# Performance work log

Hardware: AMD Instinct MI355X
Metric: run time of the kernel (lower is better)

## Reference

```python
import jax, jax.numpy as jnp
import numpy as np

B, L1, L2 = 16, 32, 128
DEC = 512       # decoder_size
MEM = 512       # memory_bank_size
TOP = 50        # topic_num


def setup_inputs() -> dict:
    key = jax.random.key(0)
    ks = jax.random.split(key, 16)
    s = lambda fan_in: 1.0 / np.sqrt(fan_in)
    inp = {
        "decoder_state": jax.random.normal(ks[0], (B, DEC), jnp.float32),
        "doc_memory": jax.random.normal(ks[1], (B, L1, MEM), jnp.float32),
        "word_memory": jax.random.normal(ks[2], (B, L1, L2, MEM), jnp.float32),
        "topic_dist": jax.random.uniform(ks[3], (B, TOP), jnp.float32),
        "doc_mask": jnp.ones((B, L1), jnp.int32),
        "word_mask": jnp.ones((B, L1, L2), jnp.int32),
        # HierAttention params (PyTorch Linear weight layout: [out, in])
        "Wv": jax.random.uniform(ks[4], (1, DEC), jnp.float32, -s(DEC), s(DEC)),
        "Wd": jax.random.uniform(ks[5], (DEC, DEC), jnp.float32, -s(DEC), s(DEC)),
        "Wt": jax.random.uniform(ks[6], (DEC, TOP), jnp.float32, -s(TOP), s(TOP)),
        "Wm": jax.random.uniform(ks[7], (DEC, MEM), jnp.float32, -s(MEM), s(MEM)),
        # doc_attention (inner Attention) params
        "Wv2": jax.random.uniform(ks[8], (1, DEC), jnp.float32, -s(DEC), s(DEC)),
        "Wd2": jax.random.uniform(ks[9], (DEC, DEC), jnp.float32, -s(DEC), s(DEC)),
        "Wt2": jax.random.uniform(ks[10], (DEC, TOP), jnp.float32, -s(TOP), s(TOP)),
        "Wm2": jax.random.uniform(ks[11], (DEC, MEM), jnp.float32, -s(MEM), s(MEM)),
    }
    return inp


def reference(decoder_state, doc_memory, word_memory, topic_dist,
              doc_mask, word_mask,
              Wv, Wd, Wt, Wm, Wv2, Wd2, Wt2, Wm2):
    neg_inf = jnp.float32(-jnp.inf)

    # ---- word-level (HierAttention.score) ----
    enc_feat = jnp.einsum('bqwm,dm->bqwd', word_memory, Wm)      # [B,L1,L2,DEC]
    dec_feat = decoder_state @ Wd.T                              # [B,DEC]
    top_feat = topic_dist @ Wt.T                                 # [B,DEC]
    e = jnp.tanh(enc_feat + (dec_feat + top_feat)[:, None, None, :])
    word_scores = jnp.einsum('bqwd,od->bqw', e, Wv)[..., 0] if Wv.shape[0] != 1 else jnp.einsum('bqwd,d->bqw', e, Wv[0])
    word_scores = jnp.where(word_mask == 0, neg_inf, word_scores)
    word_attn = jax.nn.softmax(word_scores, axis=-1)             # [B,L1,L2]

    # ---- doc-level (Attention.score) ----
    enc_feat_d = jnp.einsum('bqm,dm->bqd', doc_memory, Wm2)      # [B,L1,DEC]
    dec_feat_d = decoder_state @ Wd2.T                           # [B,DEC]
    top_feat_d = topic_dist @ Wt2.T                              # [B,DEC]
    e_d = jnp.tanh(enc_feat_d + (dec_feat_d + top_feat_d)[:, None, :])
    doc_scores = jnp.einsum('bqd,d->bq', e_d, Wv2[0])            # [B,L1]
    doc_scores = jnp.where(doc_mask == 0, neg_inf, doc_scores)
    doc_attn = jax.nn.softmax(doc_scores, axis=-1)               # [B,L1]

    # ---- combine ----
    rescaled = doc_attn[..., None] * word_attn                   # [B,L1,L2]
    context = jnp.einsum('bqw,bqwm->bm', rescaled, word_memory)  # [B,MEM]
    return context, rescaled
```

## Files before the change

### kernel.cpp

```cpp
#include <hip/hip_runtime.h>
#include <hip/hip_bf16.h>
#include <math.h>

#define BATCH 16
#define L1 32
#define L2 128
#define DEC 512
#define MEM 512
#define TOPN 50
#define NROWS (BATCH * L1 * L2)
#define NBQ (BATCH * L1)

typedef short short8 __attribute__((ext_vector_type(8)));
typedef float f32x16 __attribute__((ext_vector_type(16)));

#define WS_WP     0
#define WS_BIAS1  262144
#define WS_BIAS2  270336
#define WS_DOCSC  278528

__device__ __forceinline__ unsigned int pkbf(float a, float b) {
    __hip_bfloat162 h = __float22bfloat162_rn(float2{a, b});
    union { __hip_bfloat162 h; unsigned int u; } c{h};
    return c.u;
}

__device__ __forceinline__ float fast_tanh(float x) {
    return 1.f - 2.f / (__expf(2.f * x) + 1.f);
}

__device__ __forceinline__ float wave_sum64(float v) {
    v += __shfl_xor(v, 1);
    v += __shfl_xor(v, 2);
    v += __shfl_xor(v, 4);
    v += __shfl_xor(v, 8);
    v += __shfl_xor(v, 16);
    v += __shfl_xor(v, 32);
    return v;
}

__global__ __launch_bounds__(256) void setup_kernel(
    const float* __restrict__ Wm,
    unsigned short* __restrict__ Wp,
    const float* __restrict__ dec, const float* __restrict__ topic,
    const float* __restrict__ Wd, const float* __restrict__ Wt,
    const float* __restrict__ Wd2, const float* __restrict__ Wt2,
    float* __restrict__ bias1, float* __restrict__ bias2,
    float* __restrict__ ctx_out)
{
    const int bid = blockIdx.x;
    const int tid = threadIdx.x;
    if (bid < 128) {
        int s = bid * 256 + tid;
        int C = s >> 10;
        int u = s & 1023;
        int nt = u >> 6, k8 = (u >> 5) & 1, n_in = u & 31;
        int d = nt * 32 + n_in;
        int k = C * 16 + k8 * 8;

        const float4* src = (const float4*)(Wm + (size_t)d * DEC + k);
        float4 v0 = src[0], v1 = src[1];
        uint4 v;
        v.x = pkbf(v0.x, v0.y); v.y = pkbf(v0.z, v0.w);
        v.z = pkbf(v1.x, v1.y); v.w = pkbf(v1.z, v1.w);
        ((uint4*)Wp)[s] = v;
    } else if (bid < 128 + 4096) {
        int gw = (bid - 128) * 4 + (tid >> 6);
        int lane = tid & 63;
        int mat = gw >> 13;
        int rem = gw & 8191;
        int bb = rem >> 9;
        int d = rem & 511;

        const float* wrow = (mat ? Wd2 : Wd) + (size_t)d * DEC;
        const float* drow = dec + (size_t)bb * DEC;
        float4 a0 = ((const float4*)wrow)[lane * 2];
        float4 a1 = ((const float4*)wrow)[lane * 2 + 1];
        float4 x0 = ((const float4*)drow)[lane * 2];
        float4 x1 = ((const float4*)drow)[lane * 2 + 1];
        float acc = a0.x * x0.x;
        acc = fmaf(a0.y, x0.y, acc);
        acc = fmaf(a0.z, x0.z, acc);
        acc = fmaf(a0.w, x0.w, acc);
        acc = fmaf(a1.x, x1.x, acc);
        acc = fmaf(a1.y, x1.y, acc);
        acc = fmaf(a1.z, x1.z, acc);
        acc = fmaf(a1.w, x1.w, acc);
        const float* trow = (mat ? Wt2 : Wt) + (size_t)d * TOPN;
        if (lane < TOPN) acc = fmaf(trow[lane], topic[bb * TOPN + lane], acc);
#pragma unroll
        for (int o = 1; o <= 32; o <<= 1) acc += __shfl_xor(acc, o);
        if (lane == 0) (mat ? bias2 : bias1)[bb * DEC + d] = acc;
    } else {
        int i = (bid - (128 + 4096)) * 256 + tid;
        float4 z = {0.f, 0.f, 0.f, 0.f};
        ((float4*)ctx_out)[i * 2] = z;
        ((float4*)ctx_out)[i * 2 + 1] = z;
    }
}

__global__ __launch_bounds__(512) void doc_score_kernel(
    const float* __restrict__ Xd,
    const float* __restrict__ Wm2,
    const float* __restrict__ Wv2,
    const float* __restrict__ bias2,
    float* __restrict__ doc_scores)
{
    __shared__ float wsum[2][8];
    const int tid = threadIdx.x;
    const int lane = tid & 63;
    const int w = tid >> 6;
    const int row0 = blockIdx.x * 2;
    const int b = row0 >> 5;

    const float4* X0 = (const float4*)(Xd + (size_t)row0 * MEM) + lane * 2;
    const float4* X1 = (const float4*)(Xd + (size_t)(row0 + 1) * MEM) + lane * 2;
    float4 xa0 = X0[0], xb0 = X0[1];
    float4 xa1 = X1[0], xb1 = X1[1];

    float s0 = 0.f, s1 = 0.f;
#pragma unroll 2
    for (int dd = 0; dd < 64; dd += 2) {
        const int d = w * 64 + dd;
        const float4* W0 = (const float4*)(Wm2 + (size_t)d * MEM) + lane * 2;
        const float4* W1 = (const float4*)(Wm2 + (size_t)(d + 1) * MEM) + lane * 2;
        float4 wa0 = W0[0], wb0 = W0[1];
        float4 wa1 = W1[0], wb1 = W1[1];

        float p00 = wa0.x * xa0.x, p01 = wa1.x * xa0.x;
        float p10 = wa0.x * xa1.x, p11 = wa1.x * xa1.x;
        p00 = fmaf(wa0.y, xa0.y, p00); p01 = fmaf(wa1.y, xa0.y, p01);
        p10 = fmaf(wa0.y, xa1.y, p10); p11 = fmaf(wa1.y, xa1.y, p11);
        p00 = fmaf(wa0.z, xa0.z, p00); p01 = fmaf(wa1.z, xa0.z, p01);
        p10 = fmaf(wa0.z, xa1.z, p10); p11 = fmaf(wa1.z, xa1.z, p11);
        p00 = fmaf(wa0.w, xa0.w, p00); p01 = fmaf(wa1.w, xa0.w, p01);
        p10 = fmaf(wa0.w, xa1.w, p10); p11 = fmaf(wa1.w, xa1.w, p11);
        p00 = fmaf(wb0.x, xb0.x, p00); p01 = fmaf(wb1.x, xb0.x, p01);
        p10 = fmaf(wb0.x, xb1.x, p10); p11 = fmaf(wb1.x, xb1.x, p11);
        p00 = fmaf(wb0.y, xb0.y, p00); p01 = fmaf(wb1.y, xb0.y, p01);
        p10 = fmaf(wb0.y, xb1.y, p10); p11 = fmaf(wb1.y, xb1.y, p11);
        p00 = fmaf(wb0.z, xb0.z, p00); p01 = fmaf(wb1.z, xb0.z, p01);
        p10 = fmaf(wb0.z, xb1.z, p10); p11 = fmaf(wb1.z, xb1.z, p11);
        p00 = fmaf(wb0.w, xb0.w, p00); p01 = fmaf(wb1.w, xb0.w, p01);
        p10 = fmaf(wb0.w, xb1.w, p10); p11 = fmaf(wb1.w, xb1.w, p11);

        p00 = wave_sum64(p00);
        p01 = wave_sum64(p01);
        p10 = wave_sum64(p10);
        p11 = wave_sum64(p11);
        if (lane == 0) {
            float wva = Wv2[d], wvb = Wv2[d + 1];
            float bsa = bias2[b * DEC + d], bsb = bias2[b * DEC + d + 1];
            s0 += fmaf(wva, fast_tanh(p00 + bsa), wvb * fast_tanh(p01 + bsb));
            s1 += fmaf(wva, fast_tanh(p10 + bsa), wvb * fast_tanh(p11 + bsb));
        }
    }
    if (lane == 0) { wsum[0][w] = s0; wsum[1][w] = s1; }
    __syncthreads();
    if (tid < 2) {
        float s = 0.f;
#pragma unroll
        for (int i = 0; i < 8; ++i) s += wsum[tid][i];
        doc_scores[row0 + tid] = s;
    }
}

__global__ __launch_bounds__(512) void fused_word_kernel(
    const float* __restrict__ X,
    const unsigned short* __restrict__ Wp,
    const float* __restrict__ Wv,
    const float* __restrict__ bias1,
    const float* __restrict__ doc_scores,
    const int* __restrict__ doc_mask,
    const int* __restrict__ word_mask,
    float* __restrict__ rescaled_out,
    float* __restrict__ ctx_out)
{
    __shared__ __align__(16) short lsA[2 * 2048];
    __shared__ float red[8][128];
    __shared__ float sS[128];
    __shared__ float rmax2[2], rsum2[2];
    __shared__ float s_dattn;
    __shared__ __align__(16) float4 part[3 * 128];

    const int tid = threadIdx.x;
    const int lane = tid & 63;
    const int wid = tid >> 6;
    const int bq = blockIdx.x;
    const int r0 = bq * L2;
    const int b = bq >> 5;
    const int q = bq & 31;

    if (tid < 32) {
        int di = b * 32 + tid;
        float dsv = doc_scores[di];
        if (doc_mask[di] == 0) dsv = -INFINITY;
        float mx = dsv;
#pragma unroll
        for (int o = 1; o <= 16; o <<= 1) mx = fmaxf(mx, __shfl_xor(mx, o));
        float e = __expf(dsv - mx);
        float sum = e;
#pragma unroll
        for (int o = 1; o <= 16; o <<= 1) sum += __shfl_xor(sum, o);
        if (tid == q) s_dattn = e / sum;
    }

    const int row = tid >> 2;
    const int kq = tid & 3;
    const int mt_s = row >> 5;
    const int rl_s = row & 31;
    const int k8_s = kq >> 1;
    const int q4 = (kq & 1) * 4;
    const int slot_s = mt_s * 64 + k8_s * 32 + rl_s;
    const float4* xs = (const float4*)(X + (size_t)(r0 + row) * DEC) + kq;

    const uint4* Bp = (const uint4*)Wp;
    const int boff = wid * 128 + lane;

    f32x16 acc[8];
#pragma unroll
    for (int t = 0; t < 8; ++t)
        acc[t] = (f32x16){0.f,0.f,0.f,0.f, 0.f,0.f,0.f,0.f, 0.f,0.f,0.f,0.f, 0.f,0.f,0.f,0.f};

    const short8* lA = (const short8*)lsA;

    float4 va[4];
#pragma unroll
    for (int i = 0; i < 4; ++i) va[i] = xs[i * 4];
    uint4 ub0[2], ub1[2];
#pragma unroll
    for (int i = 0; i < 2; ++i) {
        ub0[i] = Bp[i * 1024 + boff];
        ub1[i] = Bp[i * 1024 + boff + 64];
    }

#pragma unroll
    for (int c = 0; c < 32; ++c) {
        const int p = c & 1;
        const int ia = c & 3;
        uint2 w2;
        w2.x = pkbf(va[ia].x, va[ia].y);
        w2.y = pkbf(va[ia].z, va[ia].w);
        *(uint2*)&lsA[(p * 256 + slot_s) * 8 + q4] = w2;
        __syncthreads();

        va[ia] = xs[((c + 4) & 31) * 4];
        uint4 nb0 = Bp[((c + 2) & 31) * 1024 + boff];
        uint4 nb1 = Bp[((c + 2) & 31) * 1024 + boff + 64];

        short8 a0 = lA[p * 256 + 0 * 64 + lane];
        short8 a1 = lA[p * 256 + 1 * 64 + lane];
        short8 a2 = lA[p * 256 + 2 * 64 + lane];
        short8 a3 = lA[p * 256 + 3 * 64 + lane];
        union { uint4 u; short8 s; } cb0{ub0[p]}, cb1{ub1[p]};
        acc[0] = __builtin_amdgcn_mfma_f32_32x32x16_bf16(a0, cb0.s, acc[0], 0, 0, 0);
        acc[1] = __builtin_amdgcn_mfma_f32_32x32x16_bf16(a0, cb1.s, acc[1], 0, 0, 0);
        acc[2] = __builtin_amdgcn_mfma_f32_32x32x16_bf16(a1, cb0.s, acc[2], 0, 0, 0);
        acc[3] = __builtin_amdgcn_mfma_f32_32x32x16_bf16(a1, cb1.s, acc[3], 0, 0, 0);
        acc[4] = __builtin_amdgcn_mfma_f32_32x32x16_bf16(a2, cb0.s, acc[4], 0, 0, 0);
        acc[5] = __builtin_amdgcn_mfma_f32_32x32x16_bf16(a2, cb1.s, acc[5], 0, 0, 0);
        acc[6] = __builtin_amdgcn_mfma_f32_32x32x16_bf16(a3, cb0.s, acc[6], 0, 0, 0);
        acc[7] = __builtin_amdgcn_mfma_f32_32x32x16_bf16(a3, cb1.s, acc[7], 0, 0, 0);

        ub0[p] = nb0; ub1[p] = nb1;
    }

    const int col = lane & 31;
    const int h = lane >> 5;
    float wv0, wv1, bs0, bs1;
    {
        int d0 = wid * 64 + col;
        int d1 = wid * 64 + 32 + col;
        wv0 = Wv[d0]; wv1 = Wv[d1];
        bs0 = bias1[b * DEC + d0]; bs1 = bias1[b * DEC + d1];
    }
#pragma unroll
    for (int mt = 0; mt < 4; ++mt) {
#pragma unroll
        for (int r = 0; r < 16; ++r) {
            float p = fmaf(wv0, fast_tanh(acc[mt * 2 + 0][r] + bs0),
                           wv1 * fast_tanh(acc[mt * 2 + 1][r] + bs1));
            p += __shfl_xor(p, 16);
            p += __shfl_xor(p, 8);
            p += __shfl_xor(p, 4);
            p += __shfl_xor(p, 2);
            p += __shfl_xor(p, 1);
            if (col == r) {
                int row_in = (r & 3) + 8 * (r >> 2) + 4 * h;
                red[wid][mt * 32 + row_in] = p;
            }
        }
    }
    __syncthreads();

    float e = 0.f, sv = 0.f;
    if (tid < 128) {
        sv = red[0][tid] + red[1][tid] + red[2][tid] + red[3][tid]
           + red[4][tid] + red[5][tid] + red[6][tid] + red[7][tid];
        if (word_mask[r0 + tid] == 0) sv = -INFINITY;
        float mx = sv;
#pragma unroll
        for (int o = 1; o <= 32; o <<= 1) mx = fmaxf(mx, __shfl_xor(mx, o));
        if (lane == 0) rmax2[wid] = mx;
    }
    __syncthreads();
    if (tid < 128) {
        float mx = fmaxf(rmax2[0], rmax2[1]);
        e = __expf(sv - mx);
        float sum = e;
#pragma unroll
        for (int o = 1; o <= 32; o <<= 1) sum += __shfl_xor(sum, o);
        if (lane == 0) rsum2[wid] = sum;
    }
    __syncthreads();
    if (tid < 128) {
        float sum = rsum2[0] + rsum2[1];
        float resc = s_dattn * (e / sum);
        sS[tid] = resc;
        rescaled_out[r0 + tid] = resc;
    }
    __syncthreads();

    const int hh = tid >> 7;
    const int m4 = tid & 127;
    const float4* Xr = (const float4*)X + (size_t)r0 * 128 + (size_t)hh * 32 * 128 + m4;
    float4 a = {0.f, 0.f, 0.f, 0.f};
#pragma unroll 8
    for (int i = 0; i < 32; ++i) {
        float rr = sS[hh * 32 + i];
        float4 v = Xr[(size_t)i * 128];
        a.x = fmaf(rr, v.x, a.x);
        a.y = fmaf(rr, v.y, a.y);
        a.z = fmaf(rr, v.z, a.z);
        a.w = fmaf(rr, v.w, a.w);
    }
    if (hh) part[(hh - 1) * 128 + m4] = a;
    __syncthreads();
    if (hh == 0) {
        float4 p0 = part[m4], p1 = part[128 + m4], p2 = part[256 + m4];
        a.x += p0.x + p1.x + p2.x;
        a.y += p0.y + p1.y + p2.y;
        a.z += p0.z + p1.z + p2.z;
        a.w += p0.w + p1.w + p2.w;
        float* dst = ctx_out + (size_t)b * MEM + m4 * 4;
        atomicAdd(dst + 0, a.x);
        atomicAdd(dst + 1, a.y);
        atomicAdd(dst + 2, a.z);
        atomicAdd(dst + 3, a.w);
    }
}

extern "C" void kernel_launch(void* const* d_in, const int* in_sizes, int n_in,
                              void* d_out, int out_size, void* d_ws, size_t ws_size,
                              hipStream_t stream) {
    const float* decoder_state = (const float*)d_in[0];
    const float* doc_memory    = (const float*)d_in[1];
    const float* word_memory   = (const float*)d_in[2];
    const float* topic_dist    = (const float*)d_in[3];
    const int*   doc_mask      = (const int*)d_in[4];
    const int*   word_mask     = (const int*)d_in[5];
    const float* Wv  = (const float*)d_in[6];
    const float* Wd  = (const float*)d_in[7];
    const float* Wt  = (const float*)d_in[8];
    const float* Wm  = (const float*)d_in[9];
    const float* Wv2 = (const float*)d_in[10];
    const float* Wd2 = (const float*)d_in[11];
    const float* Wt2 = (const float*)d_in[12];
    const float* Wm2 = (const float*)d_in[13];

    float* ws = (float*)d_ws;
    unsigned short* Wp  = (unsigned short*)(ws + WS_WP);
    float* bias1       = ws + WS_BIAS1;
    float* bias2       = ws + WS_BIAS2;
    float* doc_scores  = ws + WS_DOCSC;

    float* ctx_out      = (float*)d_out;
    float* rescaled_out = (float*)d_out + BATCH * MEM;

    setup_kernel<<<128 + 4096 + 4, 256, 0, stream>>>(Wm, Wp,
                                                     decoder_state, topic_dist,
                                                     Wd, Wt, Wd2, Wt2, bias1, bias2, ctx_out);
    doc_score_kernel<<<256, 512, 0, stream>>>(doc_memory, Wm2, Wv2, bias2, doc_scores);
    fused_word_kernel<<<NBQ, 512, 0, stream>>>(word_memory, Wp, Wv, bias1,
                                               doc_scores, doc_mask, word_mask,
                                               rescaled_out, ctx_out);
}
```

Before: 312.4 us.

## Switch bias and doc-score GEMVs from wave-per-output to thread-per-output

The bias GEMV in setup_kernel and the doc-score projection now give each thread a whole output row, with the shared input vector staged in LDS, instead of giving each wave one output and reducing with cross-lane shuffles. This shrinks the setup grid from over 4000 blocks to a few hundred and removes the per-output shuffle reductions. In exchange, each thread walks a strided weight row on its own, so global loads are no longer coalesced across lanes, and there is far less parallelism to hide latency.

```diff
diff --git a/kernel.cpp b/kernel.cpp
--- a/kernel.cpp
+++ b/kernel.cpp
@@ -27,16 +27,6 @@
 
 __device__ __forceinline__ float fast_tanh(float x) {
     return 1.f - 2.f / (__expf(2.f * x) + 1.f);
-}
-
-__device__ __forceinline__ float wave_sum64(float v) {
-    v += __shfl_xor(v, 1);
-    v += __shfl_xor(v, 2);
-    v += __shfl_xor(v, 4);
-    v += __shfl_xor(v, 8);
-    v += __shfl_xor(v, 16);
-    v += __shfl_xor(v, 32);
-    return v;
 }
 
 __global__ __launch_bounds__(256) void setup_kernel(
@@ -64,103 +54,104 @@
         v.x = pkbf(v0.x, v0.y); v.y = pkbf(v0.z, v0.w);
         v.z = pkbf(v1.x, v1.y); v.w = pkbf(v1.z, v1.w);
         ((uint4*)Wp)[s] = v;
-    } else if (bid < 128 + 4096) {
-        int gw = (bid - 128) * 4 + (tid >> 6);
-        int lane = tid & 63;
-        int mat = gw >> 13;
-        int rem = gw & 8191;
-        int bb = rem >> 9;
-        int d = rem & 511;
+    } else if (bid < 128 + 64) {
+        __shared__ float sdec[DEC];
+        __shared__ float stop[TOPN];
+        const int u = bid - 128;
+        const int mat = u >> 5;
+        const int bb = (u >> 1) & 15;
+        const int half = u & 1;
+        const int d = half * 256 + tid;
+
+        if (tid < 128) {
+            float4 v = ((const float4*)(dec + (size_t)bb * DEC))[tid];
+            ((float4*)sdec)[tid] = v;
+        }
+        if (tid >= 128 && tid < 128 + TOPN) stop[tid - 128] = topic[bb * TOPN + (tid - 128)];
+        __syncthreads();
 
         const float* wrow = (mat ? Wd2 : Wd) + (size_t)d * DEC;
-        const float* drow = dec + (size_t)bb * DEC;
-        float4 a0 = ((const float4*)wrow)[lane * 2];
-        float4 a1 = ((const float4*)wrow)[lane * 2 + 1];
-        float4 x0 = ((const float4*)drow)[lane * 2];
-        float4 x1 = ((const float4*)drow)[lane * 2 + 1];
-        float acc = a0.x * x0.x;
-        acc = fmaf(a0.y, x0.y, acc);
-        acc = fmaf(a0.z, x0.z, acc);
-        acc = fmaf(a0.w, x0.w, acc);
-        acc = fmaf(a1.x, x1.x, acc);
-        acc = fmaf(a1.y, x1.y, acc);
-        acc = fmaf(a1.z, x1.z, acc);
-        acc = fmaf(a1.w, x1.w, acc);
+        float acc = 0.f;
+#pragma unroll 8
+        for (int k4 = 0; k4 < 128; ++k4) {
+            float4 w = ((const float4*)wrow)[k4];
+            float4 x = ((const float4*)sdec)[k4];
+            acc = fmaf(w.x, x.x, acc);
+            acc = fmaf(w.y, x.y, acc);
+            acc = fmaf(w.z, x.z, acc);
+            acc = fmaf(w.w, x.w, acc);
+        }
         const float* trow = (mat ? Wt2 : Wt) + (size_t)d * TOPN;
-        if (lane < TOPN) acc = fmaf(trow[lane], topic[bb * TOPN + lane], acc);
-#pragma unroll
-        for (int o = 1; o <= 32; o <<= 1) acc += __shfl_xor(acc, o);
-        if (lane == 0) (mat ? bias2 : bias1)[bb * DEC + d] = acc;
+#pragma unroll 5
+        for (int t2 = 0; t2 < TOPN / 2; ++t2) {
+            float2 w = ((const float2*)trow)[t2];
+            acc = fmaf(w.x, stop[t2 * 2], acc);
+            acc = fmaf(w.y, stop[t2 * 2 + 1], acc);
+        }
+        (mat ? bias2 : bias1)[bb * DEC + d] = acc;
     } else {
-        int i = (bid - (128 + 4096)) * 256 + tid;
+        int i = (bid - (128 + 64)) * 256 + tid;
         float4 z = {0.f, 0.f, 0.f, 0.f};
         ((float4*)ctx_out)[i * 2] = z;
         ((float4*)ctx_out)[i * 2 + 1] = z;
     }
 }
 
-__global__ __launch_bounds__(512) void doc_score_kernel(
+__global__ __launch_bounds__(256) void doc_score_kernel(
     const float* __restrict__ Xd,
     const float* __restrict__ Wm2,
     const float* __restrict__ Wv2,
     const float* __restrict__ bias2,
     float* __restrict__ doc_scores)
 {
-    __shared__ float wsum[2][8];
+    __shared__ float xrow0[MEM];
+    __shared__ float xrow1[MEM];
+    __shared__ float wsum[2][4];
     const int tid = threadIdx.x;
     const int lane = tid & 63;
     const int w = tid >> 6;
     const int row0 = blockIdx.x * 2;
     const int b = row0 >> 5;
 
-    const float4* X0 = (const float4*)(Xd + (size_t)row0 * MEM) + lane * 2;
-    const float4* X1 = (const float4*)(Xd + (size_t)(row0 + 1) * MEM) + lane * 2;
-    float4 xa0 = X0[0], xb0 = X0[1];
-    float4 xa1 = X1[0], xb1 = X1[1];
+    if (tid < 128) {
+        float4 v = ((const float4*)(Xd + (size_t)row0 * MEM))[tid];
+        ((float4*)xrow0)[tid] = v;
+    } else {
+        float4 v = ((const float4*)(Xd + (size_t)(row0 + 1) * MEM))[tid - 128];
+        ((float4*)xrow1)[tid - 128] = v;
+    }
+    __syncthreads();
 
     float s0 = 0.f, s1 = 0.f;
-#pragma unroll 2
-    for (int dd = 0; dd < 64; dd += 2) {
-        const int d = w * 64 + dd;
-        const float4* W0 = (const float4*)(Wm2 + (size_t)d * MEM) + lane * 2;
-        const float4* W1 = (const float4*)(Wm2 + (size_t)(d + 1) * MEM) + lane * 2;
-        float4 wa0 = W0[0], wb0 = W0[1];
-        float4 wa1 = W1[0], wb1 = W1[1];
-
-        float p00 = wa0.x * xa0.x, p01 = wa1.x * xa0.x;
-        float p10 = wa0.x * xa1.x, p11 = wa1.x * xa1.x;
-        p00 = fmaf(wa0.y, xa0.y, p00); p01 = fmaf(wa1.y, xa0.y, p01);
-        p10 = fmaf(wa0.y, xa1.y, p10); p11 = fmaf(wa1.y, xa1.y, p11);
-        p00 = fmaf(wa0.z, xa0.z, p00); p01 = fmaf(wa1.z, xa0.z, p01);
-        p10 = fmaf(wa0.z, xa1.z, p10); p11 = fmaf(wa1.z, xa1.z, p11);
-        p00 = fmaf(wa0.w, xa0.w, p00); p01 = fmaf(wa1.w, xa0.w, p01);
-        p10 = fmaf(wa0.w, xa1.w, p10); p11 = fmaf(wa1.w, xa1.w, p11);
-        p00 = fmaf(wb0.x, xb0.x, p00); p01 = fmaf(wb1.x, xb0.x, p01);
-        p10 = fmaf(wb0.x, xb1.x, p10); p11 = fmaf(wb1.x, xb1.x, p11);
-        p00 = fmaf(wb0.y, xb0.y, p00); p01 = fmaf(wb1.y, xb0.y, p01);
-        p10 = fmaf(wb0.y, xb1.y, p10); p11 = fmaf(wb1.y, xb1.y, p11);
-        p00 = fmaf(wb0.z, xb0.z, p00); p01 = fmaf(wb1.z, xb0.z, p01);
-        p10 = fmaf(wb0.z, xb1.z, p10); p11 = fmaf(wb1.z, xb1.z, p11);
-        p00 = fmaf(wb0.w, xb0.w, p00); p01 = fmaf(wb1.w, xb0.w, p01);
-        p10 = fmaf(wb0.w, xb1.w, p10); p11 = fmaf(wb1.w, xb1.w, p11);
-
-        p00 = wave_sum64(p00);
-        p01 = wave_sum64(p01);
-        p10 = wave_sum64(p10);
-        p11 = wave_sum64(p11);
-        if (lane == 0) {
-            float wva = Wv2[d], wvb = Wv2[d + 1];
-            float bsa = bias2[b * DEC + d], bsb = bias2[b * DEC + d + 1];
-            s0 += fmaf(wva, fast_tanh(p00 + bsa), wvb * fast_tanh(p01 + bsb));
-            s1 += fmaf(wva, fast_tanh(p10 + bsa), wvb * fast_tanh(p11 + bsb));
-        }
+#pragma unroll
+    for (int dd = 0; dd < 2; ++dd) {
+        const int d = dd * 256 + tid;
+        const float4* W = (const float4*)(Wm2 + (size_t)d * MEM);
+        float a0 = 0.f, a1 = 0.f;
+#pragma unroll 8
+        for (int k4 = 0; k4 < 128; ++k4) {
+            float4 wv = W[k4];
+            float4 x0 = ((const float4*)xrow0)[k4];
+            float4 x1 = ((const float4*)xrow1)[k4];
+            a0 = fmaf(wv.x, x0.x, a0); a1 = fmaf(wv.x, x1.x, a1);
+            a0 = fmaf(wv.y, x0.y, a0); a1 = fmaf(wv.y, x1.y, a1);
+            a0 = fmaf(wv.z, x0.z, a0); a1 = fmaf(wv.z, x1.z, a1);
+            a0 = fmaf(wv.w, x0.w, a0); a1 = fmaf(wv.w, x1.w, a1);
+        }
+        const float wvd = Wv2[d];
+        const float bsd = bias2[b * DEC + d];
+        s0 = fmaf(wvd, fast_tanh(a0 + bsd), s0);
+        s1 = fmaf(wvd, fast_tanh(a1 + bsd), s1);
+    }
+#pragma unroll
+    for (int o = 1; o <= 32; o <<= 1) {
+        s0 += __shfl_xor(s0, o);
+        s1 += __shfl_xor(s1, o);
     }
     if (lane == 0) { wsum[0][w] = s0; wsum[1][w] = s1; }
     __syncthreads();
     if (tid < 2) {
-        float s = 0.f;
-#pragma unroll
-        for (int i = 0; i < 8; ++i) s += wsum[tid][i];
+        float s = wsum[tid][0] + wsum[tid][1] + wsum[tid][2] + wsum[tid][3];
         doc_scores[row0 + tid] = s;
     }
 }
@@ -377,10 +368,10 @@
     float* ctx_out      = (float*)d_out;
     float* rescaled_out = (float*)d_out + BATCH * MEM;
 
-    setup_kernel<<<128 + 4096 + 4, 256, 0, stream>>>(Wm, Wp,
-                                                     decoder_state, topic_dist,
-                                                     Wd, Wt, Wd2, Wt2, bias1, bias2, ctx_out);
-    doc_score_kernel<<<256, 512, 0, stream>>>(doc_memory, Wm2, Wv2, bias2, doc_scores);
+    setup_kernel<<<128 + 64 + 4, 256, 0, stream>>>(Wm, Wp,
+                                                   decoder_state, topic_dist,
+                                                   Wd, Wt, Wd2, Wt2, bias1, bias2, ctx_out);
+    doc_score_kernel<<<256, 256, 0, stream>>>(doc_memory, Wm2, Wv2, bias2, doc_scores);
     fused_word_kernel<<<NBQ, 512, 0, stream>>>(word_memory, Wp, Wv, bias1,
                                                doc_scores, doc_mask, word_mask,
                                                rescaled_out, ctx_out);
```

After: 329.3 us. +5.4%, slower.
